# Kernel tuning notes

Hardware: AMD Instinct MI355X
Metric: run time of the kernel (lower is better)

The kernel has to match this reference:

```python
import jax, jax.numpy as jnp
import numpy as np
from jax import lax

V, F, B = 25000, 8192, 1024  # vertices, faces, block size (batch_size)
EPS = 1e-8

def setup_inputs() -> dict:
    key = jax.random.key(0)
    k1, k2, k3 = jax.random.split(key, 3)
    vertices = jax.random.normal(k1, (V, 3), dtype=jnp.float32)
    faces = jax.random.randint(k2, (F, 3), 0, V, dtype=jnp.int64)
    face_probs = jax.random.uniform(k3, (F,), dtype=jnp.float32)
    return {"vertices": vertices, "faces": faces, "face_probs": face_probs}

def reference(vertices, faces, face_probs):
    nF = faces.shape[0]
    # edges = cat([ (f0,f1), (f1,f2), (f2,f0) ])  -> [E,2], E = 3F
    edges = jnp.concatenate([faces[:, [0, 1]], faces[:, [1, 2]], faces[:, [2, 0]]], axis=0)
    # Faithful to source: edge_to_face = arange(F).repeat_interleave(3)
    edge_to_face = jnp.repeat(jnp.arange(nF), 3)
    edge_points = vertices[edges]              # [E,2,3]
    centroids = edge_points.mean(axis=1)       # [E,3]
    E = edges.shape[0]
    v_all = edge_points[:, 1] - edge_points[:, 0] + EPS  # edge directions + eps, [E,3]
    starts = edge_points[:, 0]                 # [E,3] (unused by count but kept for clarity)
    col_idx = jnp.arange(E)

    def block(carry, b):
        row_cnt, col_cnt = carry
        i0 = b * B
        c_blk = lax.dynamic_slice(centroids, (i0, 0), (B, 3))   # [B,3]
        v1 = lax.dynamic_slice(v_all, (i0, 0), (B, 3))          # [B,3]
        # pairwise L2 distances [B,E]
        d2 = ((c_blk[:, None, :] - centroids[None, :, :]) ** 2).sum(-1)
        dists = jnp.sqrt(d2)
        pair = (dists < 1.0 + 1e-6) & ((i0 + jnp.arange(B))[:, None] < col_idx[None, :])
        # cross2 = cross(v1, v2); crossing iff ||cross2||+eps > 1e-5
        cross2 = jnp.cross(v1[:, None, :], v_all[None, :, :])   # [B,E,3]
        norm2 = jnp.sqrt((cross2 ** 2).sum(-1)) + EPS
        # after clamp t in [0,1] always, so crossings = pair & valid
        crossings = (pair & (norm2 > 1e-5)).astype(jnp.float32)
        row_cnt = lax.dynamic_update_slice(row_cnt, crossings.sum(1), (i0,))
        col_cnt = col_cnt + crossings.sum(0)
        return (row_cnt, col_cnt), None

    init = (jnp.zeros(E, jnp.float32), jnp.zeros(E, jnp.float32))
    (row_cnt, col_cnt), _ = lax.scan(block, init, jnp.arange(E // B))
    cnt_per_edge = row_cnt + col_cnt           # times edge appears as e1 or e2 in a crossing
    crossing_count = jax.ops.segment_sum(cnt_per_edge, edge_to_face, num_segments=nF)
    crossing_count = jnp.clip(crossing_count, 0.0, 100.0)
    return (face_probs * crossing_count).mean()
```

## Files before the change

### kernel.cpp

```cpp
#include <hip/hip_runtime.h>

#define V_ 25000
#define F_ 8192
#define E_ (3 * F_)

constexpr int CAP  = 101;
constexpr int GD   = 8;
constexpr int NC   = GD*GD*GD;
constexpr int CAPC = 6144;
constexpr int FLATCAP = 384;

constexpr size_t OFF_LIST = 393216;
constexpr size_t OFF_CCNT = 50724864;
constexpr size_t OFF_CNT  = 50726912;

__device__ const int PPAT[26][3] = {
    { 1, 1, 1},
    { 1, 1, 0},{ 1, 0, 1},{ 0, 1, 1},
    { 1, 0, 0},{ 0, 1, 0},{ 0, 0, 1},{ 1, 1,-1},{ 1,-1, 1},{-1, 1, 1},
    { 1,-1, 0},{ 1, 0,-1},{ 0, 1,-1},{-1, 1, 0},{-1, 0, 1},{ 0,-1, 1},
    {-1, 0, 0},{ 0,-1, 0},{ 0, 0,-1},{-1,-1, 1},{-1, 1,-1},{ 1,-1,-1},
    {-1,-1, 0},{-1, 0,-1},{ 0,-1,-1},
    {-1,-1,-1}
};

__device__ __forceinline__ int cell_coord(float c)
{
    return min(GD-1, max(0, (int)floorf(c) + GD/2));
}

__global__ __launch_bounds__(256) void build_kernel(
    const float* __restrict__ vertices, const int* __restrict__ faces,
    float4* __restrict__ C4, float4* __restrict__ cellList,
    int* __restrict__ cellCount)
{
    __shared__ int lh[NC];
    __shared__ int lbase[NC];
    for (int i = threadIdx.x; i < NC; i += 256) lh[i] = 0;
    __syncthreads();

    const int e = blockIdx.x * 256 + threadIdx.x;
    int f, i0, i1;
    if (e < F_)        { f = e;        i0 = 0; i1 = 1; }
    else if (e < 2*F_) { f = e - F_;   i0 = 1; i1 = 2; }
    else               { f = e - 2*F_; i0 = 2; i1 = 0; }
    int a = faces[f*3 + i0];
    int b = faces[f*3 + i1];
    float cx = 0.5f*(vertices[a*3+0] + vertices[b*3+0]);
    float cy = 0.5f*(vertices[a*3+1] + vertices[b*3+1]);
    float cz = 0.5f*(vertices[a*3+2] + vertices[b*3+2]);
    int cell = (cell_coord(cz)*GD + cell_coord(cy))*GD + cell_coord(cx);
    int rank = atomicAdd(&lh[cell], 1);
    __syncthreads();
    for (int i = threadIdx.x; i < NC; i += 256) {
        int c = lh[i];
        if (c) lbase[i] = atomicAdd(&cellCount[i], c);
    }
    __syncthreads();
    C4[e] = make_float4(cx, cy, cz, __int_as_float(cell));
    cellList[(size_t)cell * CAPC + lbase[cell] + rank] = make_float4(cx, cy, cz, 0.f);
}

__global__ __launch_bounds__(256) void count_kernel(
    const float4* __restrict__ C4, const float4* __restrict__ cellList,
    const int* __restrict__ cellCount, int* __restrict__ cnt)
{
    __shared__ unsigned flatLDS[4][FLATCAP + 16];
    const int wave = threadIdx.x >> 6;
    const int lane = threadIdx.x & 63;
    const int e = blockIdx.x * 4 + wave;

    float4 s = C4[e];
    const float ex = s.x, ey = s.y, ez = s.z;
    const int   cell = __float_as_int(s.w);
    const int ix = cell & 7, iy = (cell >> 3) & 7, iz = cell >> 6;
    const float d2t = (1.0f + 1e-6f) * (1.0f + 1e-6f);

    int count = 0;

    {
        const int n = cellCount[cell];
        const float4* __restrict__ L = cellList + (size_t)cell * CAPC;
        float4 cur = L[lane];
        for (int base = 0;;) {
            int nb = base + 64;
            bool more = nb < n;
            float4 nxt;
            if (more) nxt = L[nb + lane];
            float dx = ex - cur.x, dy = ey - cur.y, dz = ez - cur.z;
            float d2 = dx*dx + dy*dy + dz*dz;
            bool c = (base + lane < n) && (d2 < d2t);
            count += __popcll(__ballot(c));
            if (count >= CAP) goto done;
            if (!more) break;
            cur = nxt; base = nb;
        }
    }

    {
        const int dirx = (ix <= 3) ? 1 : -1;
        const int diry = (iy <= 3) ? 1 : -1;
        const int dirz = (iz <= 3) ? 1 : -1;

        int cq = 0, nq = 0, cellq = cell;
        if (lane < 26) {
            int ox = PPAT[lane][0] * dirx;
            int oy = PPAT[lane][1] * diry;
            int oz = PPAT[lane][2] * dirz;
            int x = ix + ox, y = iy + oy, z = iz + oz;
            if (((unsigned)x < (unsigned)GD) & ((unsigned)y < (unsigned)GD) &
                ((unsigned)z < (unsigned)GD)) {
                cellq = cell + oz*64 + oy*8 + ox;
                nq = cellCount[cellq];
                cq = (nq + 63) >> 6;
            }
        }
        int incl = cq;
#pragma unroll
        for (int d = 1; d < 64; d <<= 1) {
            int t = __shfl_up(incl, d, 64);
            if (lane >= d) incl += t;
        }
        const int T = __shfl(incl, 63);
        const int excl = incl - cq;

        if (T == 0) goto done;

        if (T > FLATCAP) {
            for (int q = 0; q < 26; ++q) {
                int ox = PPAT[q][0] * dirx, oy = PPAT[q][1] * diry,
                    oz = PPAT[q][2] * dirz;
                int x = ix + ox, y = iy + oy, z = iz + oz;
                if (((unsigned)x >= (unsigned)GD) | ((unsigned)y >= (unsigned)GD) |
                    ((unsigned)z >= (unsigned)GD)) continue;
                int nc2 = cell + oz*64 + oy*8 + ox;
                int n = cellCount[nc2];
                const float4* __restrict__ L = cellList + (size_t)nc2 * CAPC;
                for (int base = 0; base < n; base += 64) {
                    float4 t4 = L[base + lane];
                    float dx = ex - t4.x, dy = ey - t4.y, dz = ez - t4.z;
                    float d2 = dx*dx + dy*dy + dz*dz;
                    bool c = (base + lane < n) && (d2 < d2t);
                    count += __popcll(__ballot(c));
                    if (count >= CAP) goto done;
                }
            }
            goto done;
        }

        for (int k = 0; k < cq; ++k)
            flatLDS[wave][excl + k] =
                ((unsigned)cellq << 14) | ((unsigned)k << 7)
                | (unsigned)min(64, nq - k*64);
        {
            int pi = T + lane;
            if (pi < T + 12) flatLDS[wave][pi] = (unsigned)cell << 14;
        }
        asm volatile("s_waitcnt lgkmcnt(0)" ::: "memory");

        const int Tp = (T + 3) & ~3;

#define FADDR(E) (cellList + (size_t)((E) >> 14) * CAPC + (((E) >> 7) & 127) * 64 + lane)
#define PROC(B, EN)                                                        \
        {                                                                  \
            float dx = ex - (B).x, dy = ey - (B).y, dz = ez - (B).z;       \
            float d2 = dx*dx + dy*dy + dz*dz;                              \
            bool c = (lane < (int)((EN) & 127u)) && (d2 < d2t);            \
            count += __popcll(__ballot(c));                                \
            if (count >= CAP) goto done;                                   \
        }

        unsigned e0 = flatLDS[wave][0], e1 = flatLDS[wave][1],
                 e2 = flatLDS[wave][2], e3 = flatLDS[wave][3];
        float4 b0 = *FADDR(e0), b1 = *FADDR(e1), b2 = *FADDR(e2), b3 = *FADDR(e3);
        for (int j = 0;; j += 4) {
            unsigned f0 = flatLDS[wave][j+4], f1 = flatLDS[wave][j+5],
                     f2 = flatLDS[wave][j+6], f3 = flatLDS[wave][j+7];
            float4 n0 = *FADDR(f0), n1 = *FADDR(f1),
                   n2 = *FADDR(f2), n3 = *FADDR(f3);
            PROC(b0, e0) PROC(b1, e1) PROC(b2, e2) PROC(b3, e3)
            if (j + 4 >= Tp) break;
            e0 = f0; e1 = f1; e2 = f2; e3 = f3;
            b0 = n0; b1 = n1; b2 = n2; b3 = n3;
        }
#undef FADDR
#undef PROC
    }
done:
    if (lane == 0) cnt[e] = count;
}

__global__ __launch_bounds__(1024) void reduce_kernel(
    const int* __restrict__ cnt, const float* __restrict__ probs,
    float* __restrict__ out)
{
    float local = 0.0f;
    for (int f = threadIdx.x; f < F_; f += 1024) {
        float c = (float)(cnt[f] + cnt[F_ + f] + cnt[2*F_ + f]);
        c = fminf(fmaxf(c, 0.0f), 100.0f);
        local += probs[f] * c;
    }
#pragma unroll
    for (int off = 32; off > 0; off >>= 1)
        local += __shfl_down(local, off, 64);
    __shared__ float wsum[16];
    if ((threadIdx.x & 63) == 0) wsum[threadIdx.x >> 6] = local;
    __syncthreads();
    if (threadIdx.x == 0) {
        float t = 0.0f;
#pragma unroll
        for (int w = 0; w < 16; w++) t += wsum[w];
        out[0] = t / (float)F_;
    }
}

extern "C" void kernel_launch(void* const* d_in, const int* in_sizes, int n_in,
                              void* d_out, int out_size, void* d_ws, size_t ws_size,
                              hipStream_t stream)
{
    const float* vertices = (const float*)d_in[0];
    const int*   faces    = (const int*)d_in[1];
    const float* probs    = (const float*)d_in[2];
    float* out = (float*)d_out;

    char* ws = (char*)d_ws;
    float4* C4        = (float4*)ws;
    float4* cellList  = (float4*)(ws + OFF_LIST);
    int*    cellCount = (int*)(ws + OFF_CCNT);
    int*    cnt       = (int*)(ws + OFF_CNT);

    hipMemsetAsync(cellCount, 0, NC * sizeof(int), stream);
    hipLaunchKernelGGL(build_kernel, dim3(E_ / 256), dim3(256), 0, stream,
                       vertices, faces, C4, cellList, cellCount);
    hipLaunchKernelGGL(count_kernel, dim3(E_ / 4), dim3(256), 0, stream,
                       C4, cellList, cellCount, cnt);
    hipLaunchKernelGGL(reduce_kernel, dim3(1), dim3(1024), 0, stream,
                       cnt, probs, out);
}
```

Baseline: 88.76 us.

## Fuse count and reduce kernels with persistent blocks and last-block reduction

Merges the per-edge counting kernel and the single-block reduction into one launch. A persistent grid of 256 blocks of 1024 threads loops over edges with one wave per edge, and an atomic completion counter lets the last block finish the reduction. This removes one kernel launch and the dependency gap between the two kernels. In exchange it adds grid-stride scheduling with a fixed wave count, which may balance the uneven per-edge work less well, plus an atomic/fence handshake.

After: 105.1 us. 18.4% more time.

```diff
diff --git a/kernel.cpp b/kernel.cpp
--- a/kernel.cpp
+++ b/kernel.cpp
@@ -10,9 +10,15 @@
 constexpr int CAPC = 6144;
 constexpr int FLATCAP = 384;
 
-constexpr size_t OFF_LIST = 393216;
-constexpr size_t OFF_CCNT = 50724864;
-constexpr size_t OFF_CNT  = 50726912;
+constexpr int CR_BLOCKS = 256;
+constexpr int CR_TPB    = 1024;
+constexpr int CR_WPB    = CR_TPB / 64;
+constexpr int CR_NW     = CR_BLOCKS * CR_WPB;
+
+constexpr size_t OFF_LIST  = 393216;
+constexpr size_t OFF_CCNT  = 50724864;
+constexpr size_t OFF_NDONE = OFF_CCNT + 2048;
+constexpr size_t OFF_CNT   = OFF_CCNT + 4096;
 
 __device__ const int PPAT[26][3] = {
     { 1, 1, 1},
@@ -61,15 +67,10 @@
     cellList[(size_t)cell * CAPC + lbase[cell] + rank] = make_float4(cx, cy, cz, 0.f);
 }
 
-__global__ __launch_bounds__(256) void count_kernel(
-    const float4* __restrict__ C4, const float4* __restrict__ cellList,
-    const int* __restrict__ cellCount, int* __restrict__ cnt)
-{
-    __shared__ unsigned flatLDS[4][FLATCAP + 16];
-    const int wave = threadIdx.x >> 6;
-    const int lane = threadIdx.x & 63;
-    const int e = blockIdx.x * 4 + wave;
-
+__device__ __forceinline__ int count_edge(
+    int e, const float4* __restrict__ C4, const float4* __restrict__ cellList,
+    const int* __restrict__ cellCount, unsigned* flat, int lane)
+{
     float4 s = C4[e];
     const float ex = s.x, ey = s.y, ez = s.z;
     const int   cell = __float_as_int(s.w);
@@ -149,12 +150,12 @@
         }
 
         for (int k = 0; k < cq; ++k)
-            flatLDS[wave][excl + k] =
+            flat[excl + k] =
                 ((unsigned)cellq << 14) | ((unsigned)k << 7)
                 | (unsigned)min(64, nq - k*64);
         {
             int pi = T + lane;
-            if (pi < T + 12) flatLDS[wave][pi] = (unsigned)cell << 14;
+            if (pi < T + 12) flat[pi] = (unsigned)cell << 14;
         }
         asm volatile("s_waitcnt lgkmcnt(0)" ::: "memory");
 
@@ -170,12 +171,10 @@
             if (count >= CAP) goto done;                                   \
         }
 
-        unsigned e0 = flatLDS[wave][0], e1 = flatLDS[wave][1],
-                 e2 = flatLDS[wave][2], e3 = flatLDS[wave][3];
+        unsigned e0 = flat[0], e1 = flat[1], e2 = flat[2], e3 = flat[3];
         float4 b0 = *FADDR(e0), b1 = *FADDR(e1), b2 = *FADDR(e2), b3 = *FADDR(e3);
         for (int j = 0;; j += 4) {
-            unsigned f0 = flatLDS[wave][j+4], f1 = flatLDS[wave][j+5],
-                     f2 = flatLDS[wave][j+6], f3 = flatLDS[wave][j+7];
+            unsigned f0 = flat[j+4], f1 = flat[j+5], f2 = flat[j+6], f3 = flat[j+7];
             float4 n0 = *FADDR(f0), n1 = *FADDR(f1),
                    n2 = *FADDR(f2), n3 = *FADDR(f3);
             PROC(b0, e0) PROC(b1, e1) PROC(b2, e2) PROC(b3, e3)
@@ -187,29 +186,54 @@
 #undef PROC
     }
 done:
-    if (lane == 0) cnt[e] = count;
-}
-
-__global__ __launch_bounds__(1024) void reduce_kernel(
-    const int* __restrict__ cnt, const float* __restrict__ probs,
+    return count;
+}
+
+__global__ __launch_bounds__(1024) void count_reduce_kernel(
+    const float4* __restrict__ C4, const float4* __restrict__ cellList,
+    const int* __restrict__ cellCount, int* __restrict__ cnt,
+    const float* __restrict__ probs, int* __restrict__ ndone,
     float* __restrict__ out)
 {
+    __shared__ unsigned flatLDS[CR_WPB][FLATCAP + 16];
+    __shared__ float wsum[CR_WPB];
+    __shared__ int lastFlag;
+    const int wave = threadIdx.x >> 6;
+    const int lane = threadIdx.x & 63;
+
+    for (int e = blockIdx.x * CR_WPB + wave; e < E_; e += CR_NW) {
+        int c = count_edge(e, C4, cellList, cellCount, flatLDS[wave], lane);
+        if (lane == 0) cnt[e] = c;
+    }
+    __syncthreads();
+    if (threadIdx.x == 0) {
+        __threadfence();
+        int old = __hip_atomic_fetch_add(ndone, 1, __ATOMIC_ACQ_REL,
+                                         __HIP_MEMORY_SCOPE_AGENT);
+        lastFlag = (old == CR_BLOCKS - 1);
+    }
+    __syncthreads();
+    if (!lastFlag) return;
+
+    __threadfence();
     float local = 0.0f;
-    for (int f = threadIdx.x; f < F_; f += 1024) {
-        float c = (float)(cnt[f] + cnt[F_ + f] + cnt[2*F_ + f]);
+    for (int f = threadIdx.x; f < F_; f += CR_TPB) {
+        int c0 = __hip_atomic_load(&cnt[f],        __ATOMIC_RELAXED, __HIP_MEMORY_SCOPE_AGENT);
+        int c1 = __hip_atomic_load(&cnt[F_ + f],   __ATOMIC_RELAXED, __HIP_MEMORY_SCOPE_AGENT);
+        int c2 = __hip_atomic_load(&cnt[2*F_ + f], __ATOMIC_RELAXED, __HIP_MEMORY_SCOPE_AGENT);
+        float c = (float)(c0 + c1 + c2);
         c = fminf(fmaxf(c, 0.0f), 100.0f);
         local += probs[f] * c;
     }
 #pragma unroll
     for (int off = 32; off > 0; off >>= 1)
         local += __shfl_down(local, off, 64);
-    __shared__ float wsum[16];
-    if ((threadIdx.x & 63) == 0) wsum[threadIdx.x >> 6] = local;
+    if (lane == 0) wsum[wave] = local;
     __syncthreads();
     if (threadIdx.x == 0) {
         float t = 0.0f;
 #pragma unroll
-        for (int w = 0; w < 16; w++) t += wsum[w];
+        for (int w = 0; w < CR_WPB; w++) t += wsum[w];
         out[0] = t / (float)F_;
     }
 }
@@ -227,13 +251,12 @@
     float4* C4        = (float4*)ws;
     float4* cellList  = (float4*)(ws + OFF_LIST);
     int*    cellCount = (int*)(ws + OFF_CCNT);
+    int*    ndone     = (int*)(ws + OFF_NDONE);
     int*    cnt       = (int*)(ws + OFF_CNT);
 
-    hipMemsetAsync(cellCount, 0, NC * sizeof(int), stream);
+    hipMemsetAsync(cellCount, 0, 4096, stream);
     hipLaunchKernelGGL(build_kernel, dim3(E_ / 256), dim3(256), 0, stream,
                        vertices, faces, C4, cellList, cellCount);
-    hipLaunchKernelGGL(count_kernel, dim3(E_ / 4), dim3(256), 0, stream,
-                       C4, cellList, cellCount, cnt);
-    hipLaunchKernelGGL(reduce_kernel, dim3(1), dim3(1024), 0, stream,
-                       cnt, probs, out);
-}
+    hipLaunchKernelGGL(count_reduce_kernel, dim3(CR_BLOCKS), dim3(CR_TPB), 0, stream,
+                       C4, cellList, cellCount, cnt, probs, ndone, out);
+}
```
